# Optimization experiments

Hardware: AMD Instinct MI355X
Metric: run time of the kernel (lower is better)

The kernel has to match this reference:

```python
import jax, jax.numpy as jnp
import numpy as np

B, C, H, W = 4, 64, 64, 64
RC, RS = 8, 4  # channel reduction, spatial reduction
CR = C // RC
KS = 2 * RS - 1  # 7


def _conv(x, w, b, stride, pad):
    y = jax.lax.conv_general_dilated(
        x, w, (stride, stride), [(pad, pad), (pad, pad)],
        dimension_numbers=('NCHW', 'OIHW', 'NCHW'))
    return y + b[None, :, None, None]


def setup_inputs() -> dict:
    key = jax.random.key(0)
    ks = jax.random.split(key, 13)

    def w_init(k, shape):
        fan_in = shape[1] * shape[2] * shape[3]
        return jax.random.normal(k, shape, jnp.float32) / jnp.sqrt(fan_in)

    x = jax.random.normal(ks[0], (B, C, H, W), jnp.float32)
    return {
        'x': x,
        'w1': w_init(ks[1], (CR, C, 1, 1)), 'b1': jnp.zeros((CR,), jnp.float32),
        'w2': w_init(ks[2], (CR, C, 1, 1)), 'b2': jnp.zeros((CR,), jnp.float32),
        'w3': w_init(ks[3], (C, C, 1, 1)),  'b3': jnp.zeros((C,), jnp.float32),
        'w4': w_init(ks[4], (C, C, KS, KS)), 'b4': jnp.zeros((C,), jnp.float32),
        'w5': w_init(ks[5], (C, C, KS, KS)), 'b5': jnp.zeros((C,), jnp.float32),
        'w6': w_init(ks[6], (C, C, 1, 1)),  'b6': jnp.zeros((C,), jnp.float32),
    }


def reference(x, w1, b1, w2, b2, w3, b3, w4, b4, w5, b5, w6, b6):
    gamma = 1.0
    x_ori = x
    b, c, h, w = x.shape
    n = h * w

    # ---- Block 1: spatial self-attention (SAGAN-style), N x N scores ----
    f = _conv(x, w1, b1, 1, 0).reshape(b, CR, n)   # [B, C/8, N]
    g = _conv(x, w2, b2, 1, 0).reshape(b, CR, n)   # [B, C/8, N]
    hh = _conv(x, w3, b3, 1, 0).reshape(b, c, n)   # [B, C, N]
    s = jnp.einsum('bci,bcj->bij', f, g)           # [B, N, N] = f^T g
    beta = jax.nn.softmax(s, axis=1)               # softmax over dim 1 (as in torch)
    o = jnp.einsum('bcn,bnm->bcm', hh, beta)       # [B, C, N]
    x2 = o.reshape(b, c, h, w)

    # ---- Block 2: channel attention over strided-conv features, C x C scores ----
    hp, wp = h // RS, w // RS
    npix = hp * wp
    f2 = _conv(x2, w4, b4, RS, RS - 1).reshape(b, c, npix)  # [B, C, N']
    g2 = _conv(x2, w5, b5, RS, RS - 1).reshape(b, c, npix)  # [B, C, N']
    h2 = _conv(x2, w6, b6, 1, 0).reshape(b, c, n)           # [B, C, N]
    s2 = jnp.einsum('bcn,bdn->bcd', f2, g2)                 # [B, C, C] = f g^T
    beta2 = jax.nn.softmax(s2, axis=1)
    # o[b,d,n] = sum_c h2[b,c,n] * beta2[b,c,d]
    o2 = jnp.einsum('bcn,bcd->bdn', h2, beta2).reshape(b, c, h, w)

    return gamma * o2 + x_ori
```

## Files before the change

kernel.cpp:

```cpp
#include <hip/hip_runtime.h>
#include <math.h>

#define BB 4
#define CC 64
#define CRR 8
#define NN 4096

typedef __attribute__((ext_vector_type(8))) short bf16x8;
typedef __attribute__((ext_vector_type(4))) float f32x4;

__device__ inline float bf2f(ushort u) {
    union { uint i; float f; } v; v.i = (uint)u << 16; return v.f;
}
__device__ inline ushort f2bf(float f) {
    uint u = __builtin_bit_cast(uint, f);
    u = (u + 0x7FFFu + ((u >> 16) & 1u)) >> 16;
    return (ushort)u;
}
__device__ inline uint bfpack2(float a, float b) {
    uint ua = __builtin_bit_cast(uint, a);
    uint ub = __builtin_bit_cast(uint, b);
    ua = (ua + 0x7FFFu + ((ua >> 16) & 1u)) >> 16;
    ub = (ub + 0x7FFFu + ((ub >> 16) & 1u)) & 0xFFFF0000u;
    return ua | ub;
}
__device__ inline uint pkrtz(float a, float b) {
    return __builtin_amdgcn_perm(__builtin_bit_cast(uint, b),
                                 __builtin_bit_cast(uint, a), 0x07060302u);
}
__device__ inline float fexp2(float x) {
#if __has_builtin(__builtin_amdgcn_exp2f)
    return __builtin_amdgcn_exp2f(x);
#else
    float r; asm("v_exp_f32 %0, %1" : "=v"(r) : "v"(x)); return r;
#endif
}

#define X2P_B 313600

__global__ __launch_bounds__(256) void produce_fgh(
    const float* __restrict__ x,
    const float* __restrict__ w1, const float* __restrict__ b1,
    const float* __restrict__ w2, const float* __restrict__ b2,
    const float* __restrict__ w3, const float* __restrict__ b3,
    ushort* __restrict__ fT, ushort* __restrict__ gT, ushort* __restrict__ hhb)
{
    const float LOG2E = 1.4426950408889634f;
    int t = threadIdx.x;
    int b = blockIdx.x & 3;
    int n = ((blockIdx.x >> 2) << 6) + (t & 63);
    int og = __builtin_amdgcn_readfirstlane(t >> 6);

    const float* xb = x + ((size_t)b << 18) + n;
    float xv[64];
#pragma unroll
    for (int c = 0; c < 64; ++c) xv[c] = xb[(size_t)c << 12];

    if (og == 0) {
        ushort fo[8], go[8];
#pragma unroll
        for (int k = 0; k < 8; ++k) {
            float a1 = b1[k], a2 = b2[k];
#pragma unroll
            for (int c = 0; c < 64; ++c) {
                a1 = fmaf(w1[k * 64 + c], xv[c], a1);
                a2 = fmaf(w2[k * 64 + c], xv[c], a2);
            }
            fo[k] = f2bf(a1 * LOG2E); go[k] = f2bf(a2);
        }
        uint4 fq = make_uint4((uint)fo[0] | ((uint)fo[1] << 16),
                              (uint)fo[2] | ((uint)fo[3] << 16),
                              (uint)fo[4] | ((uint)fo[5] << 16),
                              (uint)fo[6] | ((uint)fo[7] << 16));
        uint4 gq = make_uint4((uint)go[0] | ((uint)go[1] << 16),
                              (uint)go[2] | ((uint)go[3] << 16),
                              (uint)go[4] | ((uint)go[5] << 16),
                              (uint)go[6] | ((uint)go[7] << 16));
        *(uint4*)&fT[((size_t)b << 15) + (size_t)n * 8] = fq;
        *(uint4*)&gT[((size_t)b << 15) + (size_t)n * 8] = gq;
#pragma unroll
        for (int k = 0; k < 4; ++k) {
            float a = b3[k];
#pragma unroll
            for (int c = 0; c < 64; ++c) a = fmaf(w3[k * 64 + c], xv[c], a);
            hhb[((size_t)b << 18) + ((size_t)k << 12) + n] = f2bf(a);
        }
    } else {
        int c0 = og * 20 - 16;
#pragma unroll
        for (int k = 0; k < 20; ++k) {
            float a = b3[c0 + k];
#pragma unroll
            for (int c = 0; c < 64; ++c) a = fmaf(w3[(c0 + k) * 64 + c], xv[c], a);
            hhb[((size_t)b << 18) + ((size_t)(c0 + k) << 12) + n] = f2bf(a);
        }
    }
}

__global__ __launch_bounds__(256) void wtz_kernel(
    const float* __restrict__ w4, const float* __restrict__ w5,
    const float* __restrict__ w6,
    ushort* __restrict__ Wt, ushort* __restrict__ w6b, ushort* __restrict__ x2p)
{
    int bid = blockIdx.x;
    int t = threadIdx.x;
    if (bid < 128) {
        int conv = bid >> 6, co = bid & 63;
        const float* W = conv ? w5 : w4;
        for (int i = t; i < 3136; i += 256) {
            int ci = i / 49, kk = i - ci * 49;
            Wt[(((size_t)(conv * 64 + co)) * 49 + kk) * 64 + ci] = f2bf(W[co * 3136 + i]);
        }
    } else if (bid == 128) {
#pragma unroll
        for (int k = 0; k < 16; ++k) {
            int i = k * 256 + t;
            w6b[i] = f2bf(w6[i]);
        }
    } else {
        int gid = (bid - 129) * 256 + t;
        if (gid >= 4 * 804) return;
        int b = gid / 804;
        int i = gid - b * 804;
        int py, px;
        if (i < 210) { py = i / 70; px = i - py * 70; }
        else if (i < 420) { int j = i - 210; int r = j / 70; py = 67 + r; px = j - r * 70; }
        else { int j = i - 420; int r = j / 6; py = 3 + r; int c = j - r * 6; px = c < 3 ? c : 64 + c; }
        ushort* p = x2p + (size_t)b * X2P_B + (size_t)(py * 70 + px) * 64;
        uint4 z = make_uint4(0, 0, 0, 0);
#pragma unroll
        for (int k = 0; k < 8; ++k) *(uint4*)(p + k * 8) = z;
    }
}

__global__ __launch_bounds__(1024) void attn_kernel(
    const ushort* __restrict__ fT, const ushort* __restrict__ gT,
    const ushort* __restrict__ hhb, const ushort* __restrict__ w6b,
    const float* __restrict__ b6,
    ushort* __restrict__ x2p, ushort* __restrict__ h2b)
{
    __shared__ __align__(16) char smem[98304];
    ushort* hhT = (ushort*)smem;
    ushort* PstB = (ushort*)(smem + 65536);
    float* Acc = (float*)smem;
    float* Lq  = (float*)(smem + 69632);
    ushort* x2s = (ushort*)(smem + 70656);

    int t = threadIdx.x;
    int q = t >> 8, tq = t & 255;
    int l = t & 63;
    int wq = tq >> 6;
    int w16 = t >> 6;
    int ml = l & 15, g = l >> 4;
    int b = blockIdx.x & 3;
    int mt = blockIdx.x >> 2;
    int m0 = mt << 6;
    int col = m0 + wq * 16 + ml;

    const ushort* fTb = fT + ((size_t)b << 15) + (size_t)q * 8192;
    const ushort* gTb = gT + ((size_t)b << 15);
    const ushort* hhB = hhb + ((size_t)b << 18) + (q << 10);

    const bf16x8 z8 = {0, 0, 0, 0, 0, 0, 0, 0};
    const f32x4 z4 = {0.f, 0.f, 0.f, 0.f};

    bf16x8 gfrag = *(const bf16x8*)(gTb + (size_t)col * 8);
    if (g != 0) gfrag = z8;

    int sc = tq >> 2, sp = tq & 3;
    const ushort* hrowBase = hhB + (size_t)sc * 4096 + sp * 16;
    int hdst = q * 8192 + sp * 1024 + sc * 8;

    uint4 h0 = *(const uint4*)(hrowBase);
    uint4 h1 = *(const uint4*)(hrowBase + 8);
    *(uint4*)&hhT[hdst] = h0;
    *(uint4*)&hhT[hdst + 512] = h1;
    bf16x8 afc[4];
#pragma unroll
    for (int s = 0; s < 4; ++s)
        afc[s] = *(const bf16x8*)(fTb + (size_t)(16 * s + ml) * 8);

    f32x4 acc[4] = {z4, z4, z4, z4};
    float rsum = 0.f;
    int swz = (ml & 7) << 4;
    char* pbase = (char*)PstB + w16 * 2048;
    __syncthreads();

    for (int nt = 0; nt < 16; ++nt) {
        int buf = nt & 1;
        bf16x8 afn[4];
        if (nt < 15) {
            int n0 = (nt + 1) << 6;
            h0 = *(const uint4*)(hrowBase + n0);
            h1 = *(const uint4*)(hrowBase + n0 + 8);
#pragma unroll
            for (int s = 0; s < 4; ++s)
                afn[s] = *(const bf16x8*)(fTb + (size_t)(n0 + 16 * s + ml) * 8);
        }

        f32x4 Sv[4];
#pragma unroll
        for (int s = 0; s < 4; ++s)
            Sv[s] = __builtin_amdgcn_mfma_f32_16x16x32_bf16(afc[s], gfrag, z4, 0, 0, 0);

        uint plo[4], phi[4];
#pragma unroll
        for (int s = 0; s < 4; ++s) {
            float p0 = fexp2(Sv[s][0]);
            float p1 = fexp2(Sv[s][1]);
            float p2 = fexp2(Sv[s][2]);
            float p3 = fexp2(Sv[s][3]);
            rsum += (p0 + p1) + (p2 + p3);
            plo[s] = pkrtz(p0, p1);
            phi[s] = pkrtz(p2, p3);
        }

#pragma unroll
        for (int s = 0; s < 4; ++s) {
            uint off = (uint)((ml * 128 + 32 * s + 8 * g) ^ swz);
            *(uint2*)(pbase + off) = make_uint2(plo[s], phi[s]);
        }

#pragma unroll
        for (int kk = 0; kk < 2; ++kk) {
            uint off = (uint)((ml * 128 + 64 * kk + 16 * g) ^ swz);
            bf16x8 pf = *(const bf16x8*)(pbase + off);
#pragma unroll
            for (int ct = 0; ct < 4; ++ct) {
                bf16x8 hf = *(const bf16x8*)&hhT[q * 8192 + buf * 4096 + (kk * 4 + g) * 512 + (16 * ct + ml) * 8];
                acc[ct] = __builtin_amdgcn_mfma_f32_16x16x32_bf16(hf, pf, acc[ct], 0, 0, 0);
            }
        }

        if (nt < 15) {
            int nb = (nt + 1) & 1;
            *(uint4*)&hhT[hdst + nb * 4096] = h0;
            *(uint4*)&hhT[hdst + nb * 4096 + 512] = h1;
#pragma unroll
            for (int s = 0; s < 4; ++s) afc[s] = afn[s];
        }
        __syncthreads();
    }

    rsum += __shfl_xor(rsum, 16);
    rsum += __shfl_xor(rsum, 32);

    {
        float* arow = Acc + q * 4352 + (wq * 16 + ml) * 68;
#pragma unroll
        for (int ct = 0; ct < 4; ++ct)
            *(f32x4*)(arow + 16 * ct + 4 * g) = acc[ct];
        if (g == 0) Lq[q * 64 + wq * 16 + ml] = rsum;
    }
    __syncthreads();

    {
        int m = t >> 4, c0 = (t & 15) << 2;
        float Ltot = Lq[m] + Lq[64 + m] + Lq[128 + m] + Lq[192 + m];
        float rL = 1.f / Ltot;
        f32x4 v0 = *(const f32x4*)(Acc + 0 * 4352 + m * 68 + c0);
        f32x4 v1 = *(const f32x4*)(Acc + 1 * 4352 + m * 68 + c0);
        f32x4 v2 = *(const f32x4*)(Acc + 2 * 4352 + m * 68 + c0);
        f32x4 v3 = *(const f32x4*)(Acc + 3 * 4352 + m * 68 + c0);
        f32x4 v;
#pragma unroll
        for (int r = 0; r < 4; ++r)
            v[r] = ((v0[r] + v1[r]) + (v2[r] + v3[r])) * rL;
        uint2 pk = make_uint2(bfpack2(v[0], v[1]), bfpack2(v[2], v[3]));
        int px = m + 3, py = mt + 3;
        *(uint2*)(x2p + (size_t)b * X2P_B + (size_t)(py * 70 + px) * 64 + c0) = pk;
        *(uint2*)(x2s + m * 72 + c0) = pk;
    }
    __syncthreads();

    {
        int dt = w16 & 3, mq = w16 >> 2;
        f32x4 hacc = z4;
#pragma unroll
        for (int kk = 0; kk < 2; ++kk) {
            bf16x8 xf = *(const bf16x8*)(x2s + (mq * 16 + ml) * 72 + 32 * kk + 8 * g);
            bf16x8 wf = *(const bf16x8*)(w6b + (size_t)(16 * dt + ml) * 64 + 32 * kk + 8 * g);
            hacc = __builtin_amdgcn_mfma_f32_16x16x32_bf16(wf, xf, hacc, 0, 0, 0);
        }
        ushort* h2row = h2b + ((size_t)b << 18) + (m0 + mq * 16 + ml);
#pragma unroll
        for (int r = 0; r < 4; ++r) {
            int d = 16 * dt + 4 * g + r;
            h2row[(size_t)d << 12] = f2bf(hacc[r] + b6[d]);
        }
    }
}

__global__ __launch_bounds__(448) void conv7_kernel(
    const ushort* __restrict__ x2p, const ushort* __restrict__ Wt,
    const float* __restrict__ b4, const float* __restrict__ b5,
    float* __restrict__ f2, float* __restrict__ g2)
{
    __shared__ float red[7][512];
    int t = threadIdx.x;
    int l = t & 63, ky = t >> 6;
    int ml = l & 15, g = l >> 4;
    int bid = blockIdx.x;
    int bc = bid & 7;
    int sub = bid >> 3;
    int ct = sub & 3, oh = sub >> 2;
    int conv = bc & 1, b = bc >> 1;

    int co0 = ct * 16;
    const ushort* wb = Wt + (size_t)conv * 200704
                     + (size_t)(co0 + ml) * 3136 + (size_t)(ky * 7) * 64 + g * 8;
    const ushort* xbase = x2p + (size_t)b * X2P_B + g * 8;

    int pixoff[2];
#pragma unroll
    for (int s = 0; s < 2; ++s) {
        int opix = oh * 32 + s * 16 + ml;
        int oy = opix >> 4, ox = opix & 15;
        pixoff[s] = ((oy * 4 + ky) * 70 + ox * 4) * 64;
    }

    const f32x4 z4 = {0.f, 0.f, 0.f, 0.f};
    f32x4 acc[2] = {z4, z4};

#pragma unroll
    for (int kx = 0; kx < 7; ++kx) {
#pragma unroll
        for (int ci0 = 0; ci0 < 64; ci0 += 32) {
            bf16x8 av = *(const bf16x8*)(wb + kx * 64 + ci0);
#pragma unroll
            for (int s = 0; s < 2; ++s) {
                bf16x8 bv = *(const bf16x8*)(xbase + pixoff[s] + kx * 64 + ci0);
                acc[s] = __builtin_amdgcn_mfma_f32_16x16x32_bf16(av, bv, acc[s], 0, 0, 0);
            }
        }
    }

#pragma unroll
    for (int s = 0; s < 2; ++s)
#pragma unroll
        for (int r = 0; r < 4; ++r)
            red[ky][(4 * g + r) * 32 + s * 16 + ml] = acc[s][r];
    __syncthreads();

    const float* bias = conv ? b5 : b4;
    float* y = conv ? g2 : f2;
    for (int idx = t; idx < 512; idx += 448) {
        float s = red[0][idx];
        s += red[1][idx]; s += red[2][idx]; s += red[3][idx];
        s += red[4][idx]; s += red[5][idx]; s += red[6][idx];
        int co = co0 + (idx >> 5);
        int opix = oh * 32 + (idx & 31);
        y[((size_t)(b * 64 + co) << 8) + opix] = s + bias[co];
    }
}

__global__ __launch_bounds__(256) void s2_softmax_kernel(
    const float* __restrict__ f2, const float* __restrict__ g2,
    float* __restrict__ beta2)
{
    __shared__ __align__(16) float g2t[256][8];
    __shared__ __align__(16) float part[16][64][4];
    __shared__ __align__(16) float s2f[64][4];
    __shared__ float mx4[4], rs4[4];
    int t = threadIdx.x;
    int b = blockIdx.x & 3;
    int d0 = (blockIdx.x >> 2) << 2;

    {
        int dd = t & 3, n0 = (t >> 2) << 2;
        const float* gp = g2 + ((size_t)(b * 64 + d0 + dd) << 8) + n0;
        float4 v = *(const float4*)gp;
        g2t[n0 + 0][dd] = v.x; g2t[n0 + 1][dd] = v.y;
        g2t[n0 + 2][dd] = v.z; g2t[n0 + 3][dd] = v.w;
    }
    __syncthreads();

    int c0 = (t & 15) << 2, nq = t >> 4;
    float acc[4][4];
#pragma unroll
    for (int i = 0; i < 4; ++i)
#pragma unroll
        for (int j = 0; j < 4; ++j) acc[i][j] = 0.f;
    const float* fb = f2 + ((size_t)(b * 64) << 8);
#pragma unroll 4
    for (int i = 0; i < 16; ++i) {
        int n = (nq << 4) + ((i + nq) & 15);
        float4 gv = *(const float4*)&g2t[n][0];
        float fv0 = fb[(c0 + 0) * 256 + n];
        float fv1 = fb[(c0 + 1) * 256 + n];
        float fv2 = fb[(c0 + 2) * 256 + n];
        float fv3 = fb[(c0 + 3) * 256 + n];
        acc[0][0] = fmaf(fv0, gv.x, acc[0][0]); acc[0][1] = fmaf(fv0, gv.y, acc[0][1]);
        acc[0][2] = fmaf(fv0, gv.z, acc[0][2]); acc[0][3] = fmaf(fv0, gv.w, acc[0][3]);
        acc[1][0] = fmaf(fv1, gv.x, acc[1][0]); acc[1][1] = fmaf(fv1, gv.y, acc[1][1]);
        acc[1][2] = fmaf(fv1, gv.z, acc[1][2]); acc[1][3] = fmaf(fv1, gv.w, acc[1][3]);
        acc[2][0] = fmaf(fv2, gv.x, acc[2][0]); acc[2][1] = fmaf(fv2, gv.y, acc[2][1]);
        acc[2][2] = fmaf(fv2, gv.z, acc[2][2]); acc[2][3] = fmaf(fv2, gv.w, acc[2][3]);
        acc[3][0] = fmaf(fv3, gv.x, acc[3][0]); acc[3][1] = fmaf(fv3, gv.y, acc[3][1]);
        acc[3][2] = fmaf(fv3, gv.z, acc[3][2]); acc[3][3] = fmaf(fv3, gv.w, acc[3][3]);
    }
#pragma unroll
    for (int i = 0; i < 4; ++i)
        *(float4*)&part[nq][c0 + i][0] =
            make_float4(acc[i][0], acc[i][1], acc[i][2], acc[i][3]);
    __syncthreads();

    if (t < 64) {
        int c = t;
        float4 s = make_float4(0.f, 0.f, 0.f, 0.f);
#pragma unroll
        for (int q2 = 0; q2 < 16; ++q2) {
            float4 v = *(const float4*)&part[q2][c][0];
            s.x += v.x; s.y += v.y; s.z += v.z; s.w += v.w;
        }
        *(float4*)&s2f[c][0] = s;
    }
    __syncthreads();
    if (t < 4) {
        float mxv = s2f[0][t];
        for (int c = 1; c < 64; ++c) mxv = fmaxf(mxv, s2f[c][t]);
        float sm = 0.f;
        for (int c = 0; c < 64; ++c) sm += __expf(s2f[c][t] - mxv);
        mx4[t] = mxv; rs4[t] = 1.f / sm;
    }
    __syncthreads();
    {
        int c = t >> 2, dd = t & 3;
        beta2[((size_t)b << 12) + c * 64 + d0 + dd] =
            __expf(s2f[c][dd] - mx4[dd]) * rs4[dd];
    }
}

__global__ __launch_bounds__(256) void o2_residual_kernel(
    const ushort* __restrict__ h2b, const float* __restrict__ beta2,
    const float* __restrict__ x, float* __restrict__ out)
{
    __shared__ __align__(16) ushort bt[64][68];
    __shared__ __align__(16) ushort btl[64][68];
    __shared__ __align__(16) ushort hn[64][68];
    int t = threadIdx.x;
    int b = blockIdx.x & 3;
    int n0 = (blockIdx.x >> 2) << 6;
    int l = t & 63, w = t >> 6;
    int ml = l & 15, g = l >> 4;

    {
        int c = t >> 2, o16 = (t & 3) << 4;
        const float* bp = beta2 + ((size_t)b << 12) + c * 64 + o16;
#pragma unroll
        for (int i = 0; i < 16; i += 4) {
            float4 v = *(const float4*)(bp + i);
            float vv[4] = {v.x, v.y, v.z, v.w};
#pragma unroll
            for (int k = 0; k < 4; ++k) {
                ushort hi = f2bf(vv[k]);
                bt[o16 + i + k][c] = hi;
                btl[o16 + i + k][c] = f2bf(vv[k] - bf2f(hi));
            }
        }
        const ushort* hp = h2b + ((size_t)(b * 64 + c) << 12) + n0 + o16;
#pragma unroll
        for (int i = 0; i < 16; i += 8) {
            uint4 hv = *(const uint4*)(hp + i);
            const ushort* hs = (const ushort*)&hv;
#pragma unroll
            for (int k = 0; k < 8; ++k) hn[o16 + i + k][c] = hs[k];
        }
    }
    __syncthreads();

    const f32x4 z4 = {0.f, 0.f, 0.f, 0.f};
    f32x4 acc[4] = {z4, z4, z4, z4};
#pragma unroll
    for (int kk = 0; kk < 2; ++kk) {
        bf16x8 ah = *(const bf16x8*)&bt[w * 16 + ml][kk * 32 + g * 8];
        bf16x8 al = *(const bf16x8*)&btl[w * 16 + ml][kk * 32 + g * 8];
#pragma unroll
        for (int nt = 0; nt < 4; ++nt) {
            bf16x8 bv = *(const bf16x8*)&hn[nt * 16 + ml][kk * 32 + g * 8];
            acc[nt] = __builtin_amdgcn_mfma_f32_16x16x32_bf16(ah, bv, acc[nt], 0, 0, 0);
            acc[nt] = __builtin_amdgcn_mfma_f32_16x16x32_bf16(al, bv, acc[nt], 0, 0, 0);
        }
    }

#pragma unroll
    for (int nt = 0; nt < 4; ++nt)
#pragma unroll
        for (int r = 0; r < 4; ++r) {
            int d = w * 16 + g * 4 + r;
            int n = n0 + nt * 16 + ml;
            size_t o = ((size_t)(b * 64 + d) << 12) + n;
            out[o] = acc[nt][r] + x[o];
        }
}

extern "C" void kernel_launch(void* const* d_in, const int* in_sizes, int n_in,
                              void* d_out, int out_size, void* d_ws, size_t ws_size,
                              hipStream_t stream)
{
    const float* x  = (const float*)d_in[0];
    const float* w1 = (const float*)d_in[1];
    const float* b1 = (const float*)d_in[2];
    const float* w2 = (const float*)d_in[3];
    const float* b2 = (const float*)d_in[4];
    const float* w3 = (const float*)d_in[5];
    const float* b3 = (const float*)d_in[6];
    const float* w4 = (const float*)d_in[7];
    const float* b4 = (const float*)d_in[8];
    const float* w5 = (const float*)d_in[9];
    const float* b5 = (const float*)d_in[10];
    const float* w6 = (const float*)d_in[11];
    const float* b6 = (const float*)d_in[12];
    float* out = (float*)d_out;

    ushort* u = (ushort*)d_ws;
    ushort* fT  = u;
    ushort* gT  = fT + 131072;
    ushort* hhb = gT + 131072;
    ushort* x2p = hhb + 1048576;
    ushort* h2b = x2p + 1254400;
    ushort* Wt  = h2b + 1048576;
    ushort* w6b = Wt + 401408;
    float* fr    = (float*)(w6b + 4096);
    float* f2    = fr;
    float* g2    = fr + 65536;
    float* beta2 = fr + 131072;

    produce_fgh<<<256, 256, 0, stream>>>(x, w1, b1, w2, b2, w3, b3, fT, gT, hhb);
    wtz_kernel<<<142, 256, 0, stream>>>(w4, w5, w6, Wt, w6b, x2p);
    attn_kernel<<<256, 1024, 0, stream>>>(fT, gT, hhb, w6b, b6, x2p, h2b);
    conv7_kernel<<<256, 448, 0, stream>>>(x2p, Wt, b4, b5, f2, g2);
    s2_softmax_kernel<<<64, 256, 0, stream>>>(f2, g2, beta2);
    o2_residual_kernel<<<256, 256, 0, stream>>>(h2b, beta2, x, out);
}
```

Baseline: 75.44 us.

## Software-pipeline score computation one tile ahead with double-buffered P staging

Restructures the attention main loop so the S=f^T g MFMA, exp2 and P write for tile nt+1 run after the PV MFMAs of tile nt, using a double-buffered per-wave P staging area. Global prefetch of hh and f moves two tiles ahead. The goal is to overlap the exp and LDS-write latency with the accumulate MFMAs. In exchange, LDS grows from 96KB to 128KB, which may hurt occupancy, and register pressure may rise.

```diff
diff --git a/kernel.cpp b/kernel.cpp
--- a/kernel.cpp
+++ b/kernel.cpp
@@ -139,7 +139,7 @@
     const float* __restrict__ b6,
     ushort* __restrict__ x2p, ushort* __restrict__ h2b)
 {
-    __shared__ __align__(16) char smem[98304];
+    __shared__ __align__(16) char smem[131072];
     ushort* hhT = (ushort*)smem;
     ushort* PstB = (ushort*)(smem + 65536);
     float* Acc = (float*)smem;
@@ -171,39 +171,27 @@
     const ushort* hrowBase = hhB + (size_t)sc * 4096 + sp * 16;
     int hdst = q * 8192 + sp * 1024 + sc * 8;
 
+    char* pwave = (char*)PstB + w16 * 4096;
+    int swz = (ml & 7) << 4;
+
+    f32x4 acc[4] = {z4, z4, z4, z4};
+    float rsum = 0.f;
+
     uint4 h0 = *(const uint4*)(hrowBase);
     uint4 h1 = *(const uint4*)(hrowBase + 8);
     *(uint4*)&hhT[hdst] = h0;
     *(uint4*)&hhT[hdst + 512] = h1;
-    bf16x8 afc[4];
+    bf16x8 afS[4];
 #pragma unroll
     for (int s = 0; s < 4; ++s)
-        afc[s] = *(const bf16x8*)(fTb + (size_t)(16 * s + ml) * 8);
-
-    f32x4 acc[4] = {z4, z4, z4, z4};
-    float rsum = 0.f;
-    int swz = (ml & 7) << 4;
-    char* pbase = (char*)PstB + w16 * 2048;
-    __syncthreads();
-
-    for (int nt = 0; nt < 16; ++nt) {
-        int buf = nt & 1;
-        bf16x8 afn[4];
-        if (nt < 15) {
-            int n0 = (nt + 1) << 6;
-            h0 = *(const uint4*)(hrowBase + n0);
-            h1 = *(const uint4*)(hrowBase + n0 + 8);
-#pragma unroll
-            for (int s = 0; s < 4; ++s)
-                afn[s] = *(const bf16x8*)(fTb + (size_t)(n0 + 16 * s + ml) * 8);
-        }
-
+        afS[s] = *(const bf16x8*)(fTb + (size_t)(16 * s + ml) * 8);
+    __syncthreads();
+
+    {
         f32x4 Sv[4];
 #pragma unroll
         for (int s = 0; s < 4; ++s)
-            Sv[s] = __builtin_amdgcn_mfma_f32_16x16x32_bf16(afc[s], gfrag, z4, 0, 0, 0);
-
-        uint plo[4], phi[4];
+            Sv[s] = __builtin_amdgcn_mfma_f32_16x16x32_bf16(afS[s], gfrag, z4, 0, 0, 0);
 #pragma unroll
         for (int s = 0; s < 4; ++s) {
             float p0 = fexp2(Sv[s][0]);
@@ -211,20 +199,24 @@
             float p2 = fexp2(Sv[s][2]);
             float p3 = fexp2(Sv[s][3]);
             rsum += (p0 + p1) + (p2 + p3);
-            plo[s] = pkrtz(p0, p1);
-            phi[s] = pkrtz(p2, p3);
-        }
-
-#pragma unroll
-        for (int s = 0; s < 4; ++s) {
             uint off = (uint)((ml * 128 + 32 * s + 8 * g) ^ swz);
-            *(uint2*)(pbase + off) = make_uint2(plo[s], phi[s]);
-        }
+            *(uint2*)(pwave + off) = make_uint2(pkrtz(p0, p1), pkrtz(p2, p3));
+        }
+    }
+    h0 = *(const uint4*)(hrowBase + 64);
+    h1 = *(const uint4*)(hrowBase + 64 + 8);
+#pragma unroll
+    for (int s = 0; s < 4; ++s)
+        afS[s] = *(const bf16x8*)(fTb + (size_t)(64 + 16 * s + ml) * 8);
+
+    for (int nt = 0; nt < 16; ++nt) {
+        int buf = nt & 1;
+        char* prd = pwave + buf * 2048;
 
 #pragma unroll
         for (int kk = 0; kk < 2; ++kk) {
             uint off = (uint)((ml * 128 + 64 * kk + 16 * g) ^ swz);
-            bf16x8 pf = *(const bf16x8*)(pbase + off);
+            bf16x8 pf = *(const bf16x8*)(prd + off);
 #pragma unroll
             for (int ct = 0; ct < 4; ++ct) {
                 bf16x8 hf = *(const bf16x8*)&hhT[q * 8192 + buf * 4096 + (kk * 4 + g) * 512 + (16 * ct + ml) * 8];
@@ -233,11 +225,34 @@
         }
 
         if (nt < 15) {
-            int nb = (nt + 1) & 1;
+            int nb = buf ^ 1;
             *(uint4*)&hhT[hdst + nb * 4096] = h0;
             *(uint4*)&hhT[hdst + nb * 4096 + 512] = h1;
-#pragma unroll
-            for (int s = 0; s < 4; ++s) afc[s] = afn[s];
+
+            f32x4 Sv[4];
+#pragma unroll
+            for (int s = 0; s < 4; ++s)
+                Sv[s] = __builtin_amdgcn_mfma_f32_16x16x32_bf16(afS[s], gfrag, z4, 0, 0, 0);
+            char* pwr = pwave + nb * 2048;
+#pragma unroll
+            for (int s = 0; s < 4; ++s) {
+                float p0 = fexp2(Sv[s][0]);
+                float p1 = fexp2(Sv[s][1]);
+                float p2 = fexp2(Sv[s][2]);
+                float p3 = fexp2(Sv[s][3]);
+                rsum += (p0 + p1) + (p2 + p3);
+                uint off = (uint)((ml * 128 + 32 * s + 8 * g) ^ swz);
+                *(uint2*)(pwr + off) = make_uint2(pkrtz(p0, p1), pkrtz(p2, p3));
+            }
+
+            if (nt < 14) {
+                int n0 = (nt + 2) << 6;
+                h0 = *(const uint4*)(hrowBase + n0);
+                h1 = *(const uint4*)(hrowBase + n0 + 8);
+#pragma unroll
+                for (int s = 0; s < 4; ++s)
+                    afS[s] = *(const bf16x8*)(fTb + (size_t)(n0 + 16 * s + ml) * 8);
+            }
         }
         __syncthreads();
     }
```

Result: faster. 72.71 us (-3.6%).
